# Performance work log

Hardware: AMD Instinct MI355X
Metric: run time of the kernel (lower is better)

## Reference

```python
import jax, jax.numpy as jnp
import numpy as np

# pywt Wavelet('db4') decomposition filters (8 taps)
DB4_DEC_LO = np.array([-0.010597401784997278, 0.032883011666982945,
                       0.030841381835986965, -0.18703481171888114,
                       -0.027983769416983849, 0.63088076792959036,
                       0.71484657055254153, 0.23037781330885523], dtype=np.float32)
# quadrature mirror: dec_hi[k] = (-1)^(k+1) * dec_lo[F-1-k]
DB4_DEC_HI = (DB4_DEC_LO[::-1] * np.array([-1.0, 1.0] * 4, dtype=np.float32)).astype(np.float32)
LEVELS = 4


def _dwt_step(x, lo, hi):
    """One pywt.dwt level, mode='symmetric'. x: [B, L] -> (cA, cD) each [B, floor((L+F-1)/2)]."""
    F = lo.shape[0]
    # symmetric half-sample extension by F-1 on each side, then drop one sample so a
    # stride-2 VALID correlation picks the odd-indexed outputs of the full valid conv
    ext = jnp.pad(x, ((0, 0), (F - 1, F - 1)), mode='symmetric')[:, 1:]
    inp = ext[:, None, :]                                # [B, 1, Lext]
    # pywt convolves (flipped filter); lax conv is correlation, so flip filters here
    ker = jnp.stack([lo[::-1], hi[::-1]])[:, None, :]    # [2, 1, F]
    y = jax.lax.conv_general_dilated(inp, ker, window_strides=(2,), padding='VALID',
                                     dimension_numbers=('NCH', 'OIH', 'NCH'))
    return y[:, 0, :], y[:, 1, :]


def _wavedec(x, levels):
    lo = jnp.asarray(DB4_DEC_LO)
    hi = jnp.asarray(DB4_DEC_HI)
    details = []
    ca = x
    for _ in range(levels):
        ca, cd = _dwt_step(ca, lo, hi)
        details.append(cd)
    # pywt ordering: [cA_n, cD_n, cD_{n-1}, ..., cD_1]
    return [ca] + details[::-1]


def setup_inputs() -> dict:
    key = jax.random.key(0)
    kx, kw, kb = jax.random.split(key, 3)
    B, L = 4096, 4096
    x = jax.random.normal(kx, (B, L), dtype=jnp.float32)
    weights = jax.random.normal(kw, (LEVELS + 1, 1), dtype=jnp.float32)
    bias = jax.random.normal(kb, (LEVELS + 1, 1), dtype=jnp.float32)
    return {"x": x, "weights": weights, "bias": bias}


def reference(x, weights, bias):
    coeffs = _wavedec(x, LEVELS)
    # per-band learnable affine: coeff_j * w_j + b_j (w_j, b_j scalars broadcast over [B, L_j])
    out = tuple(c * weights[j, 0] + bias[j, 0] for j, c in enumerate(coeffs))
    return out
```

## Files before the change

kernel.cpp:

```cpp
#include <hip/hip_runtime.h>

#define NT 256

#define L0 -0.010597401784997278f
#define L1f 0.032883011666982945f
#define L2f 0.030841381835986965f
#define L3f -0.18703481171888114f
#define L4f -0.02798376941698385f
#define L5f 0.6308807679295904f
#define L6f 0.7148465705525415f
#define L7f 0.23037781330885523f


constexpr int B_ROWS = 4096;
constexpr int LVL1 = 4096, N1 = 2051, N2 = 1029, N3 = 518, N4 = 262;
constexpr size_t OFF_CA4 = 0;
constexpr size_t OFF_CD4 = (size_t)B_ROWS * N4;
constexpr size_t OFF_CD3 = OFF_CD4 + (size_t)B_ROWS * N4;
constexpr size_t OFF_CD2 = OFF_CD3 + (size_t)B_ROWS * N3;
constexpr size_t OFF_CD1 = OFF_CD2 + (size_t)B_ROWS * N2;

__device__ __forceinline__ void dwt_one_clamped(const float* __restrict__ src, int L, int t,
                                                float& slo, float& shi) {
    constexpr float LOR[8] = {L7f, L6f, L5f, L4f, L3f, L2f, L1f, L0};
    constexpr float HIR[8] = {L0, -L1f, L2f, -L3f, L4f, -L5f, L6f, -L7f};
    const int idx0 = 2 * t - 6;
    slo = 0.f; shi = 0.f;
#pragma unroll
    for (int m = 0; m < 8; ++m) {
        int q = idx0 + m;
        q = (q < 0) ? (-1 - q) : q;
        q = (q >= L) ? (2 * L - 1 - q) : q;
        const float v = src[q];
        slo = fmaf(LOR[m], v, slo);
        shi = fmaf(HIR[m], v, shi);
    }
}

template <bool SCALE_A>
__device__ __forceinline__ void dwt_level(const float* __restrict__ src, int L,
                                          float* __restrict__ dstA, float wa, float ba,
                                          float* __restrict__ outD, float wd, float bd) {
    constexpr float LOR[8] = {L7f, L6f, L5f, L4f, L3f, L2f, L1f, L0};
    constexpr float HIR[8] = {L0, -L1f, L2f, -L3f, L4f, -L5f, L6f, -L7f};
    const int N = (L + 7) >> 1;
    const int tmax = (L - 2) >> 1;
    const int tid = threadIdx.x;

    for (int t = 3 + tid; t <= tmax; t += NT) {
        const float2* p = reinterpret_cast<const float2*>(src + 2 * t - 6);
        const float2 a = p[0], b = p[1], c = p[2], d = p[3];
        float w0 = a.x, w1 = a.y, w2 = b.x, w3 = b.y, w4 = c.x, w5 = c.y, w6 = d.x, w7 = d.y;
        float slo, shi;
        slo = LOR[0] * w0;            shi = HIR[0] * w0;
        slo = fmaf(LOR[1], w1, slo);  shi = fmaf(HIR[1], w1, shi);
        slo = fmaf(LOR[2], w2, slo);  shi = fmaf(HIR[2], w2, shi);
        slo = fmaf(LOR[3], w3, slo);  shi = fmaf(HIR[3], w3, shi);
        slo = fmaf(LOR[4], w4, slo);  shi = fmaf(HIR[4], w4, shi);
        slo = fmaf(LOR[5], w5, slo);  shi = fmaf(HIR[5], w5, shi);
        slo = fmaf(LOR[6], w6, slo);  shi = fmaf(HIR[6], w6, shi);
        slo = fmaf(LOR[7], w7, slo);  shi = fmaf(HIR[7], w7, shi);
        dstA[t] = SCALE_A ? fmaf(wa, slo, ba) : slo;
        outD[t] = fmaf(wd, shi, bd);
    }

    if (tid < 3) {
        float slo, shi;
        dwt_one_clamped(src, L, tid, slo, shi);
        dstA[tid] = SCALE_A ? fmaf(wa, slo, ba) : slo;
        outD[tid] = fmaf(wd, shi, bd);
    }
    {
        const int t = tmax + 1 + tid;
        if (tid < 4 && t < N) {
            float slo, shi;
            dwt_one_clamped(src, L, t, slo, shi);
            dstA[t] = SCALE_A ? fmaf(wa, slo, ba) : slo;
            outD[t] = fmaf(wd, shi, bd);
        }
    }
}

__global__ __launch_bounds__(NT) void lwt_kernel(const float* __restrict__ x,
                                                 const float* __restrict__ w,
                                                 const float* __restrict__ bias,
                                                 float* __restrict__ out) {
    __shared__ __align__(16) float sA[LVL1];
    __shared__ __align__(16) float sB[N1];
    const int row = blockIdx.x;
    const int tid = threadIdx.x;

    {
        const float4* src = reinterpret_cast<const float4*>(x + (size_t)row * LVL1);
        float4* dst = reinterpret_cast<float4*>(sA);
#pragma unroll
        for (int i = 0; i < LVL1 / 4 / NT; ++i)
            dst[tid + i * NT] = src[tid + i * NT];
    }

    const float w0 = w[0], w1 = w[1], w2 = w[2], w3 = w[3], w4 = w[4];
    const float b0 = bias[0], b1 = bias[1], b2 = bias[2], b3 = bias[3], b4 = bias[4];

    float* outCD1 = out + OFF_CD1 + (size_t)row * N1;
    float* outCD2 = out + OFF_CD2 + (size_t)row * N2;
    float* outCD3 = out + OFF_CD3 + (size_t)row * N3;
    float* outCD4 = out + OFF_CD4 + (size_t)row * N4;
    float* outCA4 = out + OFF_CA4 + (size_t)row * N4;

    __syncthreads();
    dwt_level<false>(sA, LVL1, sB, 0.f, 0.f, outCD1, w4, b4);
    __syncthreads();
    dwt_level<false>(sB, N1, sA, 0.f, 0.f, outCD2, w3, b3);
    __syncthreads();
    dwt_level<false>(sA, N2, sB, 0.f, 0.f, outCD3, w2, b2);
    __syncthreads();
    dwt_level<true>(sB, N3, outCA4, w0, b0, outCD4, w1, b1);
}

extern "C" void kernel_launch(void* const* d_in, const int* in_sizes, int n_in,
                              void* d_out, int out_size, void* d_ws, size_t ws_size,
                              hipStream_t stream) {
    const float* x = (const float*)d_in[0];
    const float* wp = (const float*)d_in[1];
    const float* bp = (const float*)d_in[2];
    float* out = (float*)d_out;
    lwt_kernel<<<dim3(B_ROWS), dim3(NT), 0, stream>>>(x, wp, bp, out);
}
```

Measured before the change: 28.88 us.

## Compute first DWT level straight from global memory, shrinking shared buffers

```diff
diff --git a/kernel.cpp b/kernel.cpp
--- a/kernel.cpp
+++ b/kernel.cpp
@@ -50,20 +50,18 @@
     for (int t = 3 + tid; t <= tmax; t += NT) {
         const float2* p = reinterpret_cast<const float2*>(src + 2 * t - 6);
         const float2 a = p[0], b = p[1], c = p[2], d = p[3];
-        float w0 = a.x, w1 = a.y, w2 = b.x, w3 = b.y, w4 = c.x, w5 = c.y, w6 = d.x, w7 = d.y;
         float slo, shi;
-        slo = LOR[0] * w0;            shi = HIR[0] * w0;
-        slo = fmaf(LOR[1], w1, slo);  shi = fmaf(HIR[1], w1, shi);
-        slo = fmaf(LOR[2], w2, slo);  shi = fmaf(HIR[2], w2, shi);
-        slo = fmaf(LOR[3], w3, slo);  shi = fmaf(HIR[3], w3, shi);
-        slo = fmaf(LOR[4], w4, slo);  shi = fmaf(HIR[4], w4, shi);
-        slo = fmaf(LOR[5], w5, slo);  shi = fmaf(HIR[5], w5, shi);
-        slo = fmaf(LOR[6], w6, slo);  shi = fmaf(HIR[6], w6, shi);
-        slo = fmaf(LOR[7], w7, slo);  shi = fmaf(HIR[7], w7, shi);
+        slo = LOR[0] * a.x;            shi = HIR[0] * a.x;
+        slo = fmaf(LOR[1], a.y, slo);  shi = fmaf(HIR[1], a.y, shi);
+        slo = fmaf(LOR[2], b.x, slo);  shi = fmaf(HIR[2], b.x, shi);
+        slo = fmaf(LOR[3], b.y, slo);  shi = fmaf(HIR[3], b.y, shi);
+        slo = fmaf(LOR[4], c.x, slo);  shi = fmaf(HIR[4], c.x, shi);
+        slo = fmaf(LOR[5], c.y, slo);  shi = fmaf(HIR[5], c.y, shi);
+        slo = fmaf(LOR[6], d.x, slo);  shi = fmaf(HIR[6], d.x, shi);
+        slo = fmaf(LOR[7], d.y, slo);  shi = fmaf(HIR[7], d.y, shi);
         dstA[t] = SCALE_A ? fmaf(wa, slo, ba) : slo;
         outD[t] = fmaf(wd, shi, bd);
     }
-
     if (tid < 3) {
         float slo, shi;
         dwt_one_clamped(src, L, tid, slo, shi);
@@ -85,18 +83,11 @@
                                                  const float* __restrict__ w,
                                                  const float* __restrict__ bias,
                                                  float* __restrict__ out) {
-    __shared__ __align__(16) float sA[LVL1];
-    __shared__ __align__(16) float sB[N1];
+    __shared__ __align__(16) float P[N1];
+    __shared__ __align__(16) float Q[N2];
     const int row = blockIdx.x;
     const int tid = threadIdx.x;
-
-    {
-        const float4* src = reinterpret_cast<const float4*>(x + (size_t)row * LVL1);
-        float4* dst = reinterpret_cast<float4*>(sA);
-#pragma unroll
-        for (int i = 0; i < LVL1 / 4 / NT; ++i)
-            dst[tid + i * NT] = src[tid + i * NT];
-    }
+    const float* __restrict__ xr = x + (size_t)row * LVL1;
 
     const float w0 = w[0], w1 = w[1], w2 = w[2], w3 = w[3], w4 = w[4];
     const float b0 = bias[0], b1 = bias[1], b2 = bias[2], b3 = bias[3], b4 = bias[4];
@@ -107,14 +98,43 @@
     float* outCD4 = out + OFF_CD4 + (size_t)row * N4;
     float* outCA4 = out + OFF_CA4 + (size_t)row * N4;
 
+    {
+        constexpr float LOR[8] = {L7f, L6f, L5f, L4f, L3f, L2f, L1f, L0};
+        constexpr float HIR[8] = {L0, -L1f, L2f, -L3f, L4f, -L5f, L6f, -L7f};
+        for (int k = tid; k <= 510; k += NT) {
+            const float4* p = reinterpret_cast<const float4*>(xr + 8 * k);
+            const float4 v0 = p[0], v1 = p[1], v2 = p[2], v3 = p[3];
+            float W[16] = {v0.x, v0.y, v0.z, v0.w, v1.x, v1.y, v1.z, v1.w,
+                           v2.x, v2.y, v2.z, v2.w, v3.x, v3.y, v3.z, v3.w};
+            const int t0 = 3 + 4 * k;
+#pragma unroll
+            for (int o = 0; o < 4; ++o) {
+                float slo = LOR[0] * W[2 * o];
+                float shi = HIR[0] * W[2 * o];
+#pragma unroll
+                for (int m = 1; m < 8; ++m) {
+                    slo = fmaf(LOR[m], W[2 * o + m], slo);
+                    shi = fmaf(HIR[m], W[2 * o + m], shi);
+                }
+                P[t0 + o] = slo;
+                outCD1[t0 + o] = fmaf(w4, shi, b4);
+            }
+        }
+        if (tid < 7) {
+            const int t = (tid < 3) ? tid : (2044 + tid);
+            float slo, shi;
+            dwt_one_clamped(xr, LVL1, t, slo, shi);
+            P[t] = slo;
+            outCD1[t] = fmaf(w4, shi, b4);
+        }
+    }
+
     __syncthreads();
-    dwt_level<false>(sA, LVL1, sB, 0.f, 0.f, outCD1, w4, b4);
+    dwt_level<false>(P, N1, Q, 0.f, 0.f, outCD2, w3, b3);
     __syncthreads();
-    dwt_level<false>(sB, N1, sA, 0.f, 0.f, outCD2, w3, b3);
+    dwt_level<false>(Q, N2, P, 0.f, 0.f, outCD3, w2, b2);
     __syncthreads();
-    dwt_level<false>(sA, N2, sB, 0.f, 0.f, outCD3, w2, b2);
-    __syncthreads();
-    dwt_level<true>(sB, N3, outCA4, w0, b0, outCD4, w1, b1);
+    dwt_level<true>(P, N3, outCA4, w0, b0, outCD4, w1, b1);
 }
 
 extern "C" void kernel_launch(void* const* d_in, const int* in_sizes, int n_in,
```

Measured after the change: 28.24 us. 1.02x faster.
